# Optimization experiments

Measured on AMD Instinct MI355X. Metric: run time of the kernel, lower is better.

Reference implementation:

```python
import jax, jax.numpy as jnp
import numpy as np

N = 50000      # nodes
E = 800000     # edges
NF = 16        # nfeature_dim
H = 128        # hidden_dim
OUT = 4        # output_dim


def _edge_conv(x, edge_index, W1, b1, W2, b2, aggr):
    """PyG EdgeConv: message = MLP(cat[x_i, x_j - x_i]) per edge, aggregate at target i.
    edge_index[0]=source j, edge_index[1]=target i."""
    src, dst = edge_index[0], edge_index[1]
    xi = x[dst]                                   # [E, F]
    xj = x[src]                                   # [E, F]
    h = jnp.concatenate([xi, xj - xi], axis=-1)   # [E, 2F]
    m = jax.nn.relu(h @ W1 + b1) @ W2 + b2        # [E, H]
    if aggr == 'max':
        out = jax.ops.segment_max(m, dst, num_segments=N)
        out = jnp.where(jnp.isfinite(out), out, 0.0)  # nodes with no in-edges -> 0
    else:  # mean
        s = jax.ops.segment_sum(m, dst, num_segments=N)
        cnt = jax.ops.segment_sum(jnp.ones((m.shape[0], 1), m.dtype), dst, num_segments=N)
        out = s / jnp.maximum(cnt, 1.0)
    return out


def setup_inputs() -> dict:
    key = jax.random.key(0)
    ks = jax.random.split(key, 20)
    s = 0.05
    inp = {
        'x': jax.random.normal(ks[0], (N, NF), dtype=jnp.float32),
        'edge_attr': jax.random.uniform(ks[1], (E, 1), dtype=jnp.float32) + 0.1,
        'edge_index': jax.random.randint(ks[2], (2, E), 0, N, dtype=jnp.int64),
        # conv0: Linear(2*NF->H), Linear(H->H)
        'W01': jax.random.normal(ks[3], (2 * NF, H), dtype=jnp.float32) * s,
        'b01': jnp.zeros((H,), jnp.float32),
        'W02': jax.random.normal(ks[4], (H, H), dtype=jnp.float32) * s,
        'b02': jnp.zeros((H,), jnp.float32),
        # conv1: Linear(2*H->H), Linear(H->H)
        'W11': jax.random.normal(ks[5], (2 * H, H), dtype=jnp.float32) * s,
        'b11': jnp.zeros((H,), jnp.float32),
        'W12': jax.random.normal(ks[6], (H, H), dtype=jnp.float32) * s,
        'b12': jnp.zeros((H,), jnp.float32),
        # conv2: Linear(2*H->H), Linear(H->H)
        'W21': jax.random.normal(ks[7], (2 * H, H), dtype=jnp.float32) * s,
        'b21': jnp.zeros((H,), jnp.float32),
        'W22': jax.random.normal(ks[8], (H, H), dtype=jnp.float32) * s,
        'b22': jnp.zeros((H,), jnp.float32),
        # final fc
        'Wf': jax.random.normal(ks[9], (H, OUT), dtype=jnp.float32) * s,
        'bf': jnp.zeros((OUT,), jnp.float32),
    }
    return inp


def reference(x, edge_attr, edge_index, W01, b01, W02, b02, W11, b11, W12, b12,
              W21, b21, W22, b22, Wf, bf):
    # edge_attr is only nan-checked in the original forward; unused in math.
    # dropout_rate = 0.0 -> identity (eval-mode reference).
    h = _edge_conv(x, edge_index, W01, b01, W02, b02, 'max')
    h = jax.nn.relu(h)
    h = _edge_conv(h, edge_index, W11, b11, W12, b12, 'mean')
    h = jax.nn.relu(h)
    h = _edge_conv(h, edge_index, W21, b21, W22, b22, 'mean')
    return h @ Wf + bf  # [N, OUT]
```

## Files before the change

### kernel.cpp

```cpp
#include <hip/hip_runtime.h>
#include <stdint.h>

#define NNODES 50000
#define NEDGES 800000
#define FDIM 16
#define HDIM 128
#define NPAD 50176
#define NCH 98
#define NBLK64 782

typedef __attribute__((ext_vector_type(8))) short short8;
typedef __attribute__((ext_vector_type(4))) float f32x4;

static constexpr size_t NH  = (size_t)NNODES * HDIM;
static constexpr size_t NHB = NH * sizeof(float);

static constexpr size_t OFF_BUF0  = 0;
static constexpr size_t OFF_BUF1  = NHB;
static constexpr size_t OFF_BUF2  = 2 * NHB;
static constexpr size_t OFF_BFB   = 3 * NHB;
static constexpr size_t OFF_CNT   = OFF_BFB + NH * 2;
static constexpr size_t OFF_CUR   = OFF_CNT + NPAD * 4;
static constexpr size_t OFF_CSUM  = OFF_CUR + NPAD * 4;
static constexpr size_t OFF_COFF  = OFF_CSUM + 512;
static constexpr size_t OFF_WFOLD = OFF_COFF + 512;
static constexpr size_t OFF_BFOLD = OFF_WFOLD + 2048;
static constexpr size_t OFF_FLAG  = OFF_BFOLD + 256;
static constexpr size_t OFF_SSRC  = OFF_FLAG + 256;
static constexpr size_t OFF_SDST  = OFF_SSRC + (size_t)NEDGES * 4;
static constexpr size_t OFF_W02H  = OFF_SDST + (size_t)NEDGES * 4;
static constexpr size_t OFF_W02L  = OFF_W02H + 32768;
static constexpr size_t OFF_W12H  = OFF_W02L + 32768;
static constexpr size_t OFF_W12L  = OFF_W12H + 32768;
static constexpr size_t OFF_W11H  = OFF_W12L + 32768;
static constexpr size_t OFF_W11L  = OFF_W11H + 65536;
static constexpr size_t OFF_W21H  = OFF_W11L + 65536;
static constexpr size_t OFF_W21L  = OFF_W21H + 65536;

__device__ inline unsigned enc_f32(float m) {
  unsigned u = __float_as_uint(m);
  return (u & 0x80000000u) ? ~u : (u | 0x80000000u);
}

__device__ inline ushort bf16_rne(float v) {
  const unsigned u = __float_as_uint(v);
  return (ushort)((u + 0x7fffu + ((u >> 16) & 1u)) >> 16);
}

__device__ inline void bf16_split(float v, ushort& h, ushort& l) {
  unsigned u = __float_as_uint(v);
  unsigned hb = (u + 0x7fffu + ((u >> 16) & 1u)) & 0xffff0000u;
  h = (ushort)(hb >> 16);
  float r = v - __uint_as_float(hb);
  unsigned ur = __float_as_uint(r);
  l = (ushort)((ur + 0x7fffu + ((ur >> 16) & 1u)) >> 16);
}

__device__ inline void split8_tr(const float v[8], short8& hv, short8& lv) {
  unsigned hp[4], lp[4];
  #pragma unroll
  for (int k = 0; k < 4; ++k) {
    const unsigned u0 = __float_as_uint(v[2 * k]);
    const unsigned u1 = __float_as_uint(v[2 * k + 1]);
    const unsigned h0 = u0 & 0xffff0000u;
    const unsigned h1 = u1 & 0xffff0000u;
    const float r0 = v[2 * k]     - __uint_as_float(h0);
    const float r1 = v[2 * k + 1] - __uint_as_float(h1);
    hp[k] = h1 | (h0 >> 16);
    lp[k] = (__float_as_uint(r1) & 0xffff0000u) | (__float_as_uint(r0) >> 16);
  }
  hv = *(short8*)hp;
  lv = *(short8*)lp;
}

__global__ __launch_bounds__(256) void k_init(const int* __restrict__ raw,
                                              int* __restrict__ flag,
                                              unsigned* __restrict__ cnt) {
  const int i = blockIdx.x * 256 + threadIdx.x;
  cnt[i] = 0u;
  if (blockIdx.x == 0 && threadIdx.x == 0) {
    int is64 = 1;
    #pragma unroll
    for (int k = 1; k < 64; k += 2)
      if (raw[k] != 0) is64 = 0;
    *flag = is64;
  }
}

__global__ __launch_bounds__(256) void k_count(const int* __restrict__ raw,
                                               const int* __restrict__ flag,
                                               unsigned* __restrict__ cnt) {
  const size_t e = (size_t)blockIdx.x * 256 + threadIdx.x;
  const int d = (*flag) ? raw[2 * ((size_t)NEDGES + e)] : raw[NEDGES + e];
  atomicAdd(&cnt[d], 1u);
}

__global__ __launch_bounds__(256) void k_scan1(const unsigned* __restrict__ cnt,
                                               unsigned* __restrict__ csum) {
  __shared__ unsigned s[256];
  const int t = threadIdx.x, b = blockIdx.x;
  s[t] = cnt[b * 512 + t] + cnt[b * 512 + 256 + t];
  __syncthreads();
  for (int off = 128; off; off >>= 1) {
    if (t < off) s[t] += s[t + off];
    __syncthreads();
  }
  if (t == 0) csum[b] = s[0];
}

__global__ void k_scan2(const unsigned* __restrict__ csum,
                        unsigned* __restrict__ coff) {
  if (threadIdx.x == 0) {
    unsigned r = 0;
    for (int i = 0; i < NCH; ++i) { coff[i] = r; r += csum[i]; }
  }
}

__global__ __launch_bounds__(256) void k_scan3(const unsigned* __restrict__ cnt,
                                               const unsigned* __restrict__ coff,
                                               unsigned* __restrict__ cursor) {
  __shared__ unsigned s[256];
  const int t = threadIdx.x, b = blockIdx.x;
  const int base = b * 512;
  const unsigned c0 = cnt[base + 2 * t], c1 = cnt[base + 2 * t + 1];
  s[t] = c0 + c1;
  __syncthreads();
  for (int off = 1; off < 256; off <<= 1) {
    unsigned v = s[t];
    if (t >= off) v += s[t - off];
    __syncthreads();
    s[t] = v;
    __syncthreads();
  }
  const unsigned o = coff[b] + s[t] - (c0 + c1);
  cursor[base + 2 * t] = o;
  cursor[base + 2 * t + 1] = o + c0;
}

__global__ __launch_bounds__(256) void k_scatter(const int* __restrict__ raw,
                                                 const int* __restrict__ flag,
                                                 unsigned* __restrict__ cursor,
                                                 int* __restrict__ ssrc,
                                                 int* __restrict__ sdst) {
  const size_t e = (size_t)blockIdx.x * 256 + threadIdx.x;
  int s, d;
  if (*flag) { s = raw[2 * e]; d = raw[2 * ((size_t)NEDGES + e)]; }
  else       { s = raw[e];     d = raw[NEDGES + e]; }
  const unsigned p = atomicAdd(&cursor[d], 1u);
  ssrc[p] = s;
  sdst[p] = d;
}

__device__ inline void prepw_body(const float* __restrict__ W2,
                                  ushort* __restrict__ Whi,
                                  ushort* __restrict__ Wlo, int blk) {
  const int gid = blk * 256 + threadIdx.x;
  const int row = gid & 15;
  const int kg  = (gid >> 4) & 3;
  const int ks  = (gid >> 6) & 3;
  const int ct  = gid >> 8;
  const int col = ct * 16 + row;
  const int k0  = ks * 32 + kg * 8;
  short8 hv, lv;
  #pragma unroll
  for (int j = 0; j < 8; ++j) {
    ushort h, l;
    bf16_split(W2[(size_t)(k0 + j) * HDIM + col], h, l);
    hv[j] = (short)h; lv[j] = (short)l;
  }
  *(short8*)(Whi + (size_t)gid * 8) = hv;
  *(short8*)(Wlo + (size_t)gid * 8) = lv;
}

__device__ inline void packab_body(const float* __restrict__ W1,
                                   ushort* __restrict__ Whi,
                                   ushort* __restrict__ Wlo, int blk) {
  const int gid = blk * 256 + threadIdx.x;
  const int row = gid & 15;
  const int kg  = (gid >> 4) & 3;
  const int ks  = (gid >> 6) & 3;
  const int ct  = gid >> 8;
  const int col = ct * 16 + row;
  const int k0  = ks * 32 + kg * 8;
  short8 hv, lv;
  #pragma unroll
  for (int j = 0; j < 8; ++j) {
    const int k = k0 + j;
    float v;
    if (col < HDIM) v = W1[(size_t)k * HDIM + col] - W1[(size_t)(k + HDIM) * HDIM + col];
    else            v = W1[(size_t)(k + HDIM) * HDIM + (col - HDIM)];
    ushort h, l;
    bf16_split(v, h, l);
    hv[j] = (short)h; lv[j] = (short)l;
  }
  *(short8*)(Whi + (size_t)gid * 8) = hv;
  *(short8*)(Wlo + (size_t)gid * 8) = lv;
}

__global__ __launch_bounds__(256) void k_prep_all(
    const float* __restrict__ W02, const float* __restrict__ W12,
    const float* __restrict__ W11, const float* __restrict__ W21,
    const float* __restrict__ W22, const float* __restrict__ Wf,
    const float* __restrict__ b22, const float* __restrict__ bf,
    ushort* __restrict__ W02h, ushort* __restrict__ W02l,
    ushort* __restrict__ W12h, ushort* __restrict__ W12l,
    ushort* __restrict__ W11h, ushort* __restrict__ W11l,
    ushort* __restrict__ W21h, ushort* __restrict__ W21l,
    float* __restrict__ Wfold, float* __restrict__ bfold) {
  const int b = blockIdx.x;
  if (b < 8)       prepw_body(W02, W02h, W02l, b);
  else if (b < 16) prepw_body(W12, W12h, W12l, b - 8);
  else if (b < 32) packab_body(W11, W11h, W11l, b - 16);
  else if (b < 48) packab_body(W21, W21h, W21l, b - 32);
  else {
    const int t = (b - 48) * 256 + threadIdx.x;
    const int f = t >> 2, o = t & 3;
    float acc = 0.f;
    for (int h = 0; h < HDIM; ++h)
      acc = fmaf(W22[f * HDIM + h], Wf[h * 4 + o], acc);
    Wfold[t] = acc;
    if (t < 4) {
      float a = bf[t];
      for (int h = 0; h < HDIM; ++h) a = fmaf(b22[h], Wf[h * 4 + t], a);
      bfold[t] = a;
    }
  }
}

__global__ __launch_bounds__(256) void k_node_ab16(const float* __restrict__ x,
                                                   const float* __restrict__ W1,
                                                   const float* __restrict__ b1,
                                                   float* __restrict__ A,
                                                   ushort* __restrict__ Bb) {
  __shared__ float s_x[16 * FDIM];
  const int tid = threadIdx.x;
  const int nb = blockIdx.x * 16;
  s_x[tid] = x[(size_t)nb * FDIM + tid];
  __syncthreads();
  const int h = tid & 127;
  const int half = tid >> 7;
  float accA[8], accB[8];
  #pragma unroll
  for (int j = 0; j < 8; ++j) { accA[j] = 0.f; accB[j] = 0.f; }
  #pragma unroll 4
  for (int f = 0; f < FDIM; ++f) {
    const float wt = W1[f * HDIM + h];
    const float wb = W1[(f + FDIM) * HDIM + h];
    const float wd = wt - wb;
    #pragma unroll
    for (int j = 0; j < 8; ++j) {
      const float xv = s_x[(half * 8 + j) * FDIM + f];
      accA[j] = fmaf(xv, wd, accA[j]);
      accB[j] = fmaf(xv, wb, accB[j]);
    }
  }
  const float bias = b1[h];
  #pragma unroll
  for (int j = 0; j < 8; ++j) {
    const size_t idx = (size_t)(nb + half * 8 + j) * HDIM + h;
    A[idx] = accA[j] + bias;
    Bb[idx] = bf16_rne(accB[j]);
  }
}

__global__ __launch_bounds__(256) void k_node_ab_mfma(
    const unsigned* __restrict__ X, const ushort* __restrict__ Whi,
    const ushort* __restrict__ Wlo, const float* __restrict__ b1,
    float* __restrict__ A, ushort* __restrict__ Bb) {
  __shared__ __align__(16) ushort s_hi[64 * 128];
  __shared__ __align__(16) ushort s_lo[64 * 128];
  const int tid = threadIdx.x;
  const int nb = blockIdx.x * 64;

  #pragma unroll
  for (int it = 0; it < 4; ++it) {
    const int idx = tid + it * 256;
    const int row = idx >> 4;
    const int kg8 = idx & 15;
    const int n = nb + row;
    float v[8];
    if (n < NNODES) {
      const unsigned* p = X + (size_t)n * HDIM + kg8 * 8;
      const uint4 u0 = *(const uint4*)p;
      const uint4 u1 = *(const uint4*)(p + 4);
      const unsigned uu[8] = {u0.x, u0.y, u0.z, u0.w, u1.x, u1.y, u1.z, u1.w};
      #pragma unroll
      for (int j = 0; j < 8; ++j)
        v[j] = (uu[j] & 0x80000000u) ? __uint_as_float(uu[j] ^ 0x80000000u) : 0.f;
    } else {
      #pragma unroll
      for (int j = 0; j < 8; ++j) v[j] = 0.f;
    }
    short8 hv, lv;
    split8_tr(v, hv, lv);
    const int unit = row * 16 + (kg8 ^ (row & 15));
    *(short8*)(s_hi + unit * 8) = hv;
    *(short8*)(s_lo + unit * 8) = lv;
  }
  __syncthreads();

  const int l15 = tid & 15;
  const int l4  = (tid >> 4) & 3;
  const int w   = tid >> 6;

  f32x4 acc[4][4];
  #pragma unroll
  for (int rt = 0; rt < 4; ++rt)
    #pragma unroll
    for (int c = 0; c < 4; ++c)
      #pragma unroll
      for (int r = 0; r < 4; ++r) acc[rt][c][r] = 0.f;

  #pragma unroll
  for (int ks = 0; ks < 4; ++ks) {
    short8 wh[4], wl[4];
    #pragma unroll
    for (int ctl = 0; ctl < 4; ++ctl) {
      const int ct_g = w * 4 + ctl;
      const size_t u = ((size_t)(((ct_g * 4 + ks) * 4 + l4) * 16 + l15)) * 8;
      wh[ctl] = *(const short8*)(Whi + u);
      wl[ctl] = *(const short8*)(Wlo + u);
    }
    #pragma unroll
    for (int rt = 0; rt < 4; ++rt) {
      const int unit = (rt * 16 + l15) * 16 + ((ks * 4 + l4) ^ l15);
      const short8 ah = *(const short8*)(s_hi + unit * 8);
      const short8 al = *(const short8*)(s_lo + unit * 8);
      #pragma unroll
      for (int ctl = 0; ctl < 4; ++ctl) {
        acc[rt][ctl] = __builtin_amdgcn_mfma_f32_16x16x32_bf16(al, wh[ctl], acc[rt][ctl], 0, 0, 0);
        acc[rt][ctl] = __builtin_amdgcn_mfma_f32_16x16x32_bf16(ah, wl[ctl], acc[rt][ctl], 0, 0, 0);
        acc[rt][ctl] = __builtin_amdgcn_mfma_f32_16x16x32_bf16(ah, wh[ctl], acc[rt][ctl], 0, 0, 0);
      }
    }
  }

  #pragma unroll
  for (int ctl = 0; ctl < 4; ++ctl) {
    const int col_g = w * 64 + ctl * 16 + l15;
    if (col_g < HDIM) {
      const float bias = b1[col_g];
      #pragma unroll
      for (int rt = 0; rt < 4; ++rt)
        #pragma unroll
        for (int r = 0; r < 4; ++r) {
          const int n = nb + rt * 16 + l4 * 4 + r;
          if (n < NNODES) A[(size_t)n * HDIM + col_g] = acc[rt][ctl][r] + bias;
        }
    } else {
      const int cb = col_g - HDIM;
      #pragma unroll
      for (int rt = 0; rt < 4; ++rt)
        #pragma unroll
        for (int r = 0; r < 4; ++r) {
          const int n = nb + rt * 16 + l4 * 4 + r;
          if (n < NNODES) Bb[(size_t)n * HDIM + cb] = bf16_rne(acc[rt][ctl][r]);
        }
    }
  }
}

__global__ __launch_bounds__(256) void k_node_l2_fused(
    const float* __restrict__ S, const unsigned* __restrict__ cnt,
    const ushort* __restrict__ W12h, const ushort* __restrict__ W12l,
    const float* __restrict__ b12,
    const ushort* __restrict__ W21h, const ushort* __restrict__ W21l,
    const float* __restrict__ b21,
    float* __restrict__ A, ushort* __restrict__ Bb) {
  __shared__ __align__(16) ushort s_hi[64 * 128];
  __shared__ __align__(16) ushort s_lo[64 * 128];
  __shared__ float s_m[64 * 132];
  __shared__ float s_scale[64];
  __shared__ float s_alive[64];
  const int tid = threadIdx.x;
  const int nb = blockIdx.x * 64;
  if (tid < 64) {
    const int n = nb + tid;
    const unsigned c = (n < NNODES) ? cnt[n] : 0u;
    s_scale[tid] = c ? 1.f / (float)c : 0.f;
    s_alive[tid] = c ? 1.f : 0.f;
  }
  __syncthreads();

  #pragma unroll
  for (int it = 0; it < 4; ++it) {
    const int idx = tid + it * 256;
    const int row = idx >> 4;
    const int kg8 = idx & 15;
    const int n = nb + row;
    float v[8];
    if (n < NNODES) {
      const float sc = s_scale[row];
      const float* p = S + (size_t)n * HDIM + kg8 * 8;
      const float4 a0 = *(const float4*)p;
      const float4 a1 = *(const float4*)(p + 4);
      v[0] = a0.x * sc; v[1] = a0.y * sc; v[2] = a0.z * sc; v[3] = a0.w * sc;
      v[4] = a1.x * sc; v[5] = a1.y * sc; v[6] = a1.z * sc; v[7] = a1.w * sc;
    } else {
      #pragma unroll
      for (int j = 0; j < 8; ++j) v[j] = 0.f;
    }
    short8 hv, lv;
    split8_tr(v, hv, lv);
    const int unit = row * 16 + (kg8 ^ (row & 15));
    *(short8*)(s_hi + unit * 8) = hv;
    *(short8*)(s_lo + unit * 8) = lv;
  }
  __syncthreads();

  const int l15 = tid & 15;
  const int l4  = (tid >> 4) & 3;
  const int w   = tid >> 6;

  {
    f32x4 acc[4][2];
    #pragma unroll
    for (int rt = 0; rt < 4; ++rt)
      #pragma unroll
      for (int c = 0; c < 2; ++c)
        #pragma unroll
        for (int r = 0; r < 4; ++r) acc[rt][c][r] = 0.f;

    #pragma unroll
    for (int ks = 0; ks < 4; ++ks) {
      short8 wh[2], wl[2];
      #pragma unroll
      for (int ctl = 0; ctl < 2; ++ctl) {
        const int ct_g = w * 2 + ctl;
        const size_t u = ((size_t)(((ct_g * 4 + ks) * 4 + l4) * 16 + l15)) * 8;
        wh[ctl] = *(const short8*)(W12h + u);
        wl[ctl] = *(const short8*)(W12l + u);
      }
      #pragma unroll
      for (int rt = 0; rt < 4; ++rt) {
        const int unit = (rt * 16 + l15) * 16 + ((ks * 4 + l4) ^ l15);
        const short8 ah = *(const short8*)(s_hi + unit * 8);
        const short8 al = *(const short8*)(s_lo + unit * 8);
        #pragma unroll
        for (int ctl = 0; ctl < 2; ++ctl) {
          acc[rt][ctl] = __builtin_amdgcn_mfma_f32_16x16x32_bf16(al, wh[ctl], acc[rt][ctl], 0, 0, 0);
          acc[rt][ctl] = __builtin_amdgcn_mfma_f32_16x16x32_bf16(ah, wl[ctl], acc[rt][ctl], 0, 0, 0);
          acc[rt][ctl] = __builtin_amdgcn_mfma_f32_16x16x32_bf16(ah, wh[ctl], acc[rt][ctl], 0, 0, 0);
        }
      }
    }

    const float bb0 = b12[w * 32 + l15];
    const float bb1 = b12[w * 32 + 16 + l15];
    #pragma unroll
    for (int rt = 0; rt < 4; ++rt)
      #pragma unroll
      for (int ctl = 0; ctl < 2; ++ctl)
        #pragma unroll
        for (int r = 0; r < 4; ++r) {
          const int row = rt * 16 + l4 * 4 + r;
          s_m[row * 132 + w * 32 + ctl * 16 + l15] =
              fmaxf(acc[rt][ctl][r] + (ctl ? bb1 : bb0), 0.f) * s_alive[row];
        }
  }
  __syncthreads();

  #pragma unroll
  for (int it = 0; it < 4; ++it) {
    const int idx = tid + it * 256;
    const int row = idx >> 4;
    const int kg8 = idx & 15;
    const float* p = s_m + row * 132 + kg8 * 8;
    float v[8];
    const float4 a0 = *(const float4*)p;
    const float4 a1 = *(const float4*)(p + 4);
    v[0] = a0.x; v[1] = a0.y; v[2] = a0.z; v[3] = a0.w;
    v[4] = a1.x; v[5] = a1.y; v[6] = a1.z; v[7] = a1.w;
    short8 hv, lv;
    split8_tr(v, hv, lv);
    const int unit = row * 16 + (kg8 ^ (row & 15));
    *(short8*)(s_hi + unit * 8) = hv;
    *(short8*)(s_lo + unit * 8) = lv;
  }
  __syncthreads();

  f32x4 acc2[4][4];
  #pragma unroll
  for (int rt = 0; rt < 4; ++rt)
    #pragma unroll
    for (int c = 0; c < 4; ++c)
      #pragma unroll
      for (int r = 0; r < 4; ++r) acc2[rt][c][r] = 0.f;

  #pragma unroll
  for (int ks = 0; ks < 4; ++ks) {
    short8 wh[4], wl[4];
    #pragma unroll
    for (int ctl = 0; ctl < 4; ++ctl) {
      const int ct_g = w * 4 + ctl;
      const size_t u = ((size_t)(((ct_g * 4 + ks) * 4 + l4) * 16 + l15)) * 8;
      wh[ctl] = *(const short8*)(W21h + u);
      wl[ctl] = *(const short8*)(W21l + u);
    }
    #pragma unroll
    for (int rt = 0; rt < 4; ++rt) {
      const int unit = (rt * 16 + l15) * 16 + ((ks * 4 + l4) ^ l15);
      const short8 ah = *(const short8*)(s_hi + unit * 8);
      const short8 al = *(const short8*)(s_lo + unit * 8);
      #pragma unroll
      for (int ctl = 0; ctl < 4; ++ctl) {
        acc2[rt][ctl] = __builtin_amdgcn_mfma_f32_16x16x32_bf16(al, wh[ctl], acc2[rt][ctl], 0, 0, 0);
        acc2[rt][ctl] = __builtin_amdgcn_mfma_f32_16x16x32_bf16(ah, wl[ctl], acc2[rt][ctl], 0, 0, 0);
        acc2[rt][ctl] = __builtin_amdgcn_mfma_f32_16x16x32_bf16(ah, wh[ctl], acc2[rt][ctl], 0, 0, 0);
      }
    }
  }

  #pragma unroll
  for (int ctl = 0; ctl < 4; ++ctl) {
    const int col_g = w * 64 + ctl * 16 + l15;
    if (col_g < HDIM) {
      const float bias = b21[col_g];
      #pragma unroll
      for (int rt = 0; rt < 4; ++rt)
        #pragma unroll
        for (int r = 0; r < 4; ++r) {
          const int n = nb + rt * 16 + l4 * 4 + r;
          if (n < NNODES) A[(size_t)n * HDIM + col_g] = acc2[rt][ctl][r] + bias;
        }
    } else {
      const int cb = col_g - HDIM;
      #pragma unroll
      for (int rt = 0; rt < 4; ++rt)
        #pragma unroll
        for (int r = 0; r < 4; ++r) {
          const int n = nb + rt * 16 + l4 * 4 + r;
          if (n < NNODES) Bb[(size_t)n * HDIM + cb] = bf16_rne(acc2[rt][ctl][r]);
        }
    }
  }
}

__global__ __launch_bounds__(256) void k_edge_l0_mfma(
    const float* __restrict__ A0, const ushort* __restrict__ B0b,
    const int* __restrict__ ssrc, const int* __restrict__ sdst,
    const ushort* __restrict__ Whi, const ushort* __restrict__ Wlo,
    const float* __restrict__ b2, unsigned* __restrict__ outenc) {
  __shared__ __align__(16) char s_un[4 * 64 * 33 * 4];
  __shared__ int s_dstA[64];
  __shared__ int s_srcA[64];
  ushort* s_thi = (ushort*)s_un;
  ushort* s_tlo = (ushort*)(s_un + 16384);
  float*  s_m   = (float*)s_un;

  const int tid = threadIdx.x;
  const int eb = blockIdx.x * 64;
  if (tid < 64) s_dstA[tid] = sdst[eb + tid];
  else if (tid < 128) s_srcA[tid - 64] = ssrc[eb + tid - 64];
  __syncthreads();

  #pragma unroll
  for (int it = 0; it < 4; ++it) {
    const int idx = tid + it * 256;
    const int e = idx >> 4;
    const int kg8 = idx & 15;
    const int k0 = kg8 * 8;
    const float* ap = A0 + (size_t)s_dstA[e] * HDIM + k0;
    const ushort* bp = B0b + (size_t)s_srcA[e] * HDIM + k0;
    const float4 a0 = *(const float4*)ap;
    const float4 a1 = *(const float4*)(ap + 4);
    const short8 b8 = *(const short8*)bp;
    const float af[8] = {a0.x, a0.y, a0.z, a0.w, a1.x, a1.y, a1.z, a1.w};
    float v[8];
    #pragma unroll
    for (int j = 0; j < 8; ++j) {
      const float bv = __uint_as_float(((unsigned)(ushort)b8[j]) << 16);
      v[j] = fmaxf(af[j] + bv, 0.f);
    }
    short8 hv, lv;
    split8_tr(v, hv, lv);
    const int unit = e * 16 + (kg8 ^ (e & 15));
    *(short8*)(s_thi + unit * 8) = hv;
    *(short8*)(s_tlo + unit * 8) = lv;
  }
  __syncthreads();

  const int l15 = tid & 15;
  const int l4  = (tid >> 4) & 3;
  const int w   = tid >> 6;

  f32x4 acc[4][2];
  #pragma unroll
  for (int rt = 0; rt < 4; ++rt)
    #pragma unroll
    for (int c = 0; c < 2; ++c)
      #pragma unroll
      for (int r = 0; r < 4; ++r) acc[rt][c][r] = 0.f;

  #pragma unroll
  for (int ks = 0; ks < 4; ++ks) {
    short8 wh[2], wl[2];
    #pragma unroll
    for (int ctl = 0; ctl < 2; ++ctl) {
      const int ct_g = w * 2 + ctl;
      const size_t u = ((size_t)(((ct_g * 4 + ks) * 4 + l4) * 16 + l15)) * 8;
      wh[ctl] = *(const short8*)(Whi + u);
      wl[ctl] = *(const short8*)(Wlo + u);
    }
    #pragma unroll
    for (int rt = 0; rt < 4; ++rt) {
      const int e = rt * 16 + l15;
      const int unit = e * 16 + ((ks * 4 + l4) ^ l15);
      const short8 ah = *(const short8*)(s_thi + unit * 8);
      const short8 al = *(const short8*)(s_tlo + unit * 8);
      #pragma unroll
      for (int ctl = 0; ctl < 2; ++ctl) {
        acc[rt][ctl] = __builtin_amdgcn_mfma_f32_16x16x32_bf16(al, wh[ctl], acc[rt][ctl], 0, 0, 0);
        acc[rt][ctl] = __builtin_amdgcn_mfma_f32_16x16x32_bf16(ah, wl[ctl], acc[rt][ctl], 0, 0, 0);
        acc[rt][ctl] = __builtin_amdgcn_mfma_f32_16x16x32_bf16(ah, wh[ctl], acc[rt][ctl], 0, 0, 0);
      }
    }
  }
  __syncthreads();

  const float bb0 = b2[w * 32 + l15];
  const float bb1 = b2[w * 32 + 16 + l15];
  float* sm = s_m + w * (64 * 33);
  #pragma unroll
  for (int rt = 0; rt < 4; ++rt)
    #pragma unroll
    for (int ctl = 0; ctl < 2; ++ctl)
      #pragma unroll
      for (int r = 0; r < 4; ++r)
        sm[(rt * 16 + l4 * 4 + r) * 33 + ctl * 16 + l15] =
            acc[rt][ctl][r] + (ctl ? bb1 : bb0);
  __syncthreads();

  {
    const int l = tid & 63;
    const int col = l & 31;
    const int g = l >> 5;
    const int e0 = g * 32;
    int curd = s_dstA[e0];
    float run = sm[e0 * 33 + col];
    for (int e = e0 + 1; e < e0 + 32; ++e) {
      const int d = s_dstA[e];
      const float v = sm[e * 33 + col];
      if (d == curd) run = fmaxf(run, v);
      else {
        atomicMax(outenc + (size_t)curd * HDIM + w * 32 + col, enc_f32(run));
        curd = d; run = v;
      }
    }
    atomicMax(outenc + (size_t)curd * HDIM + w * 32 + col, enc_f32(run));
  }
}

__global__ __launch_bounds__(256) void k_seg_mean(const float* __restrict__ A,
                                                  const ushort* __restrict__ B,
                                                  const int* __restrict__ ssrc,
                                                  const unsigned* __restrict__ endv,
                                                  const unsigned* __restrict__ cnt,
                                                  float* __restrict__ S) {
  const int tid = threadIdx.x;
  const int n = blockIdx.x * 4 + (tid >> 6);
  const int lane = tid & 63;
  const unsigned end = endv[n];
  unsigned e = end - cnt[n];
  const float2 a = *(const float2*)(A + (size_t)n * HDIM + lane * 2);
  float sx = 0.f, sy = 0.f;
  for (; e + 8 <= end; e += 8) {
    int s[8];
    #pragma unroll
    for (int k = 0; k < 8; ++k) s[k] = ssrc[e + k];
    unsigned bv[8];
    #pragma unroll
    for (int k = 0; k < 8; ++k)
      bv[k] = *(const unsigned*)(B + (size_t)s[k] * HDIM + lane * 2);
    #pragma unroll
    for (int k = 0; k < 8; ++k) {
      sx += fmaxf(a.x + __uint_as_float(bv[k] << 16), 0.f);
      sy += fmaxf(a.y + __uint_as_float(bv[k] & 0xffff0000u), 0.f);
    }
  }
  for (; e < end; ++e) {
    const unsigned bv = *(const unsigned*)(B + (size_t)ssrc[e] * HDIM + lane * 2);
    sx += fmaxf(a.x + __uint_as_float(bv << 16), 0.f);
    sy += fmaxf(a.y + __uint_as_float(bv & 0xffff0000u), 0.f);
  }
  float2 o; o.x = sx; o.y = sy;
  *(float2*)(S + (size_t)n * HDIM + lane * 2) = o;
}

__global__ __launch_bounds__(256) void k_seg_final(const float* __restrict__ A,
                                                   const ushort* __restrict__ B,
                                                   const int* __restrict__ ssrc,
                                                   const unsigned* __restrict__ endv,
                                                   const unsigned* __restrict__ cnt,
                                                   const float* __restrict__ Wfold,
                                                   const float* __restrict__ bfold,
                                                   const float* __restrict__ bf,
                                                   float* __restrict__ out) {
  const int tid = threadIdx.x;
  const int n = blockIdx.x * 4 + (tid >> 6);
  const int lane = tid & 63;
  const unsigned deg = cnt[n];
  if (deg == 0) {
    if (lane == 0) {
      float4 o; o.x = bf[0]; o.y = bf[1]; o.z = bf[2]; o.w = bf[3];
      ((float4*)out)[n] = o;
    }
    return;
  }
  const unsigned end = endv[n];
  unsigned e = end - deg;
  const float2 a = *(const float2*)(A + (size_t)n * HDIM + lane * 2);
  float sx = 0.f, sy = 0.f;
  for (; e + 8 <= end; e += 8) {
    int s[8];
    #pragma unroll
    for (int k = 0; k < 8; ++k) s[k] = ssrc[e + k];
    unsigned bv[8];
    #pragma unroll
    for (int k = 0; k < 8; ++k)
      bv[k] = *(const unsigned*)(B + (size_t)s[k] * HDIM + lane * 2);
    #pragma unroll
    for (int k = 0; k < 8; ++k) {
      sx += fmaxf(a.x + __uint_as_float(bv[k] << 16), 0.f);
      sy += fmaxf(a.y + __uint_as_float(bv[k] & 0xffff0000u), 0.f);
    }
  }
  for (; e < end; ++e) {
    const unsigned bv = *(const unsigned*)(B + (size_t)ssrc[e] * HDIM + lane * 2);
    sx += fmaxf(a.x + __uint_as_float(bv << 16), 0.f);
    sy += fmaxf(a.y + __uint_as_float(bv & 0xffff0000u), 0.f);
  }
  const float inv = 1.f / (float)deg;
  const float vx = sx * inv, vy = sy * inv;
  const float4 w0 = ((const float4*)Wfold)[lane * 2];
  const float4 w1 = ((const float4*)Wfold)[lane * 2 + 1];
  float p0 = fmaf(vx, w0.x, vy * w1.x);
  float p1 = fmaf(vx, w0.y, vy * w1.y);
  float p2 = fmaf(vx, w0.z, vy * w1.z);
  float p3 = fmaf(vx, w0.w, vy * w1.w);
  #pragma unroll
  for (int off = 32; off; off >>= 1) {
    p0 += __shfl_xor(p0, off);
    p1 += __shfl_xor(p1, off);
    p2 += __shfl_xor(p2, off);
    p3 += __shfl_xor(p3, off);
  }
  if (lane == 0) {
    float4 o;
    o.x = p0 + bfold[0]; o.y = p1 + bfold[1];
    o.z = p2 + bfold[2]; o.w = p3 + bfold[3];
    ((float4*)out)[n] = o;
  }
}

extern "C" void kernel_launch(void* const* d_in, const int* in_sizes, int n_in,
                              void* d_out, int out_size, void* d_ws, size_t ws_size,
                              hipStream_t stream) {
  const float* x   = (const float*)d_in[0];
  const int*   eidx = (const int*)d_in[2];
  const float* W01 = (const float*)d_in[3];
  const float* b01 = (const float*)d_in[4];
  const float* W02 = (const float*)d_in[5];
  const float* b02 = (const float*)d_in[6];
  const float* W11 = (const float*)d_in[7];
  const float* b11 = (const float*)d_in[8];
  const float* W12 = (const float*)d_in[9];
  const float* b12 = (const float*)d_in[10];
  const float* W21 = (const float*)d_in[11];
  const float* b21 = (const float*)d_in[12];
  const float* W22 = (const float*)d_in[13];
  const float* b22 = (const float*)d_in[14];
  const float* Wf  = (const float*)d_in[15];
  const float* bf  = (const float*)d_in[16];
  float* out = (float*)d_out;
  char* ws = (char*)d_ws;

  float* buf0 = (float*)(ws + OFF_BUF0);
  float* buf1 = (float*)(ws + OFF_BUF1);
  float* buf2 = (float*)(ws + OFF_BUF2);
  ushort* bufB = (ushort*)(ws + OFF_BFB);
  unsigned* cnt    = (unsigned*)(ws + OFF_CNT);
  unsigned* cursor = (unsigned*)(ws + OFF_CUR);
  unsigned* csum   = (unsigned*)(ws + OFF_CSUM);
  unsigned* coff   = (unsigned*)(ws + OFF_COFF);
  float* Wfold = (float*)(ws + OFF_WFOLD);
  float* bfold = (float*)(ws + OFF_BFOLD);
  int* flag  = (int*)(ws + OFF_FLAG);
  int* ssrc  = (int*)(ws + OFF_SSRC);
  int* sdst  = (int*)(ws + OFF_SDST);
  ushort* W02h = (ushort*)(ws + OFF_W02H);
  ushort* W02l = (ushort*)(ws + OFF_W02L);
  ushort* W12h = (ushort*)(ws + OFF_W12H);
  ushort* W12l = (ushort*)(ws + OFF_W12L);
  ushort* W11h = (ushort*)(ws + OFF_W11H);
  ushort* W11l = (ushort*)(ws + OFF_W11L);
  ushort* W21h = (ushort*)(ws + OFF_W21H);
  ushort* W21l = (ushort*)(ws + OFF_W21L);

  k_init<<<NPAD / 256, 256, 0, stream>>>(eidx, flag, cnt);
  k_count<<<NEDGES / 256, 256, 0, stream>>>(eidx, flag, cnt);
  k_scan1<<<NCH, 256, 0, stream>>>(cnt, csum);
  k_scan2<<<1, 64, 0, stream>>>(csum, coff);
  k_scan3<<<NCH, 256, 0, stream>>>(cnt, coff, cursor);
  k_scatter<<<NEDGES / 256, 256, 0, stream>>>(eidx, flag, cursor, ssrc, sdst);
  k_prep_all<<<50, 256, 0, stream>>>(W02, W12, W11, W21, W22, Wf, b22, bf,
                                     W02h, W02l, W12h, W12l, W11h, W11l,
                                     W21h, W21l, Wfold, bfold);

  k_node_ab16<<<NNODES / 16, 256, 0, stream>>>(x, W01, b01, buf0, bufB);
  hipMemsetAsync(buf2, 0, NHB, stream);
  k_edge_l0_mfma<<<NEDGES / 64, 256, 0, stream>>>(buf0, bufB, ssrc, sdst,
                                                  W02h, W02l, b02, (unsigned*)buf2);

  k_node_ab_mfma<<<NBLK64, 256, 0, stream>>>((const unsigned*)buf2, W11h, W11l,
                                             b11, buf0, bufB);
  k_seg_mean<<<NNODES / 4, 256, 0, stream>>>(buf0, bufB, ssrc, cursor, cnt, buf1);

  k_node_l2_fused<<<NBLK64, 256, 0, stream>>>(buf1, cnt, W12h, W12l, b12,
                                              W21h, W21l, b21, buf0, bufB);
  k_seg_final<<<NNODES / 4, 256, 0, stream>>>(buf0, bufB, ssrc, cursor, cnt,
                                              Wfold, bfold, bf, out);

  (void)in_sizes; (void)n_in; (void)out_size; (void)ws_size;
}
```

Baseline: 468.3 us.

## Use single-pass bf16 MFMA in layer-0 edge kernel, fuse memset, deepen gather unroll

The layer-0 edge MLP second matmul drops the split hi/lo bf16 three-MFMA emulation of fp32 and uses one bf16 MFMA, with activations converted by a packed bf16 convert instruction. This cuts MFMA work and shared-memory traffic to a third but lowers precision of the max-aggregated messages. The separate memset of the max-aggregation buffer is folded into the init kernel, and the mean-aggregation gather loops are unrolled from 8 to 16 edges, with a 4-edge remainder step in one of them.

```diff
diff --git a/kernel.cpp b/kernel.cpp
--- a/kernel.cpp
+++ b/kernel.cpp
@@ -73,12 +73,22 @@
   lv = *(short8*)lp;
 }
 
+__device__ inline short8 cvtpk8_bf16(const float v[8]) {
+  unsigned r[4];
+  #pragma unroll
+  for (int k = 0; k < 4; ++k)
+    asm("v_cvt_pk_bf16_f32 %0, %1, %2" : "=v"(r[k]) : "v"(v[2 * k]), "v"(v[2 * k + 1]));
+  return *(short8*)r;
+}
+
 __global__ __launch_bounds__(256) void k_init(const int* __restrict__ raw,
                                               int* __restrict__ flag,
-                                              unsigned* __restrict__ cnt) {
+                                              unsigned* __restrict__ cnt,
+                                              unsigned* __restrict__ outenc) {
   const int i = blockIdx.x * 256 + threadIdx.x;
-  cnt[i] = 0u;
-  if (blockIdx.x == 0 && threadIdx.x == 0) {
+  outenc[i] = 0u;
+  if (i < NPAD) cnt[i] = 0u;
+  if (i == 0) {
     int is64 = 1;
     #pragma unroll
     for (int k = 1; k < 64; k += 2)
@@ -539,14 +549,13 @@
 __global__ __launch_bounds__(256) void k_edge_l0_mfma(
     const float* __restrict__ A0, const ushort* __restrict__ B0b,
     const int* __restrict__ ssrc, const int* __restrict__ sdst,
-    const ushort* __restrict__ Whi, const ushort* __restrict__ Wlo,
+    const ushort* __restrict__ Whi,
     const float* __restrict__ b2, unsigned* __restrict__ outenc) {
   __shared__ __align__(16) char s_un[4 * 64 * 33 * 4];
   __shared__ int s_dstA[64];
   __shared__ int s_srcA[64];
-  ushort* s_thi = (ushort*)s_un;
-  ushort* s_tlo = (ushort*)(s_un + 16384);
-  float*  s_m   = (float*)s_un;
+  ushort* s_t = (ushort*)s_un;
+  float*  s_m = (float*)s_un;
 
   const int tid = threadIdx.x;
   const int eb = blockIdx.x * 64;
@@ -572,11 +581,9 @@
       const float bv = __uint_as_float(((unsigned)(ushort)b8[j]) << 16);
       v[j] = fmaxf(af[j] + bv, 0.f);
     }
-    short8 hv, lv;
-    split8_tr(v, hv, lv);
+    const short8 hv = cvtpk8_bf16(v);
     const int unit = e * 16 + (kg8 ^ (e & 15));
-    *(short8*)(s_thi + unit * 8) = hv;
-    *(short8*)(s_tlo + unit * 8) = lv;
+    *(short8*)(s_t + unit * 8) = hv;
   }
   __syncthreads();
 
@@ -594,26 +601,21 @@
 
   #pragma unroll
   for (int ks = 0; ks < 4; ++ks) {
-    short8 wh[2], wl[2];
+    short8 wh[2];
     #pragma unroll
     for (int ctl = 0; ctl < 2; ++ctl) {
       const int ct_g = w * 2 + ctl;
       const size_t u = ((size_t)(((ct_g * 4 + ks) * 4 + l4) * 16 + l15)) * 8;
       wh[ctl] = *(const short8*)(Whi + u);
-      wl[ctl] = *(const short8*)(Wlo + u);
     }
     #pragma unroll
     for (int rt = 0; rt < 4; ++rt) {
       const int e = rt * 16 + l15;
       const int unit = e * 16 + ((ks * 4 + l4) ^ l15);
-      const short8 ah = *(const short8*)(s_thi + unit * 8);
-      const short8 al = *(const short8*)(s_tlo + unit * 8);
-      #pragma unroll
-      for (int ctl = 0; ctl < 2; ++ctl) {
-        acc[rt][ctl] = __builtin_amdgcn_mfma_f32_16x16x32_bf16(al, wh[ctl], acc[rt][ctl], 0, 0, 0);
-        acc[rt][ctl] = __builtin_amdgcn_mfma_f32_16x16x32_bf16(ah, wl[ctl], acc[rt][ctl], 0, 0, 0);
+      const short8 ah = *(const short8*)(s_t + unit * 8);
+      #pragma unroll
+      for (int ctl = 0; ctl < 2; ++ctl)
         acc[rt][ctl] = __builtin_amdgcn_mfma_f32_16x16x32_bf16(ah, wh[ctl], acc[rt][ctl], 0, 0, 0);
-      }
     }
   }
   __syncthreads();
@@ -664,16 +666,30 @@
   unsigned e = end - cnt[n];
   const float2 a = *(const float2*)(A + (size_t)n * HDIM + lane * 2);
   float sx = 0.f, sy = 0.f;
-  for (; e + 8 <= end; e += 8) {
-    int s[8];
-    #pragma unroll
-    for (int k = 0; k < 8; ++k) s[k] = ssrc[e + k];
-    unsigned bv[8];
-    #pragma unroll
-    for (int k = 0; k < 8; ++k)
+  for (; e + 16 <= end; e += 16) {
+    int s[16];
+    #pragma unroll
+    for (int k = 0; k < 16; ++k) s[k] = ssrc[e + k];
+    unsigned bv[16];
+    #pragma unroll
+    for (int k = 0; k < 16; ++k)
       bv[k] = *(const unsigned*)(B + (size_t)s[k] * HDIM + lane * 2);
     #pragma unroll
-    for (int k = 0; k < 8; ++k) {
+    for (int k = 0; k < 16; ++k) {
+      sx += fmaxf(a.x + __uint_as_float(bv[k] << 16), 0.f);
+      sy += fmaxf(a.y + __uint_as_float(bv[k] & 0xffff0000u), 0.f);
+    }
+  }
+  for (; e + 4 <= end; e += 4) {
+    int s[4];
+    #pragma unroll
+    for (int k = 0; k < 4; ++k) s[k] = ssrc[e + k];
+    unsigned bv[4];
+    #pragma unroll
+    for (int k = 0; k < 4; ++k)
+      bv[k] = *(const unsigned*)(B + (size_t)s[k] * HDIM + lane * 2);
+    #pragma unroll
+    for (int k = 0; k < 4; ++k) {
       sx += fmaxf(a.x + __uint_as_float(bv[k] << 16), 0.f);
       sy += fmaxf(a.y + __uint_as_float(bv[k] & 0xffff0000u), 0.f);
     }
@@ -711,16 +727,16 @@
   unsigned e = end - deg;
   const float2 a = *(const float2*)(A + (size_t)n * HDIM + lane * 2);
   float sx = 0.f, sy = 0.f;
-  for (; e + 8 <= end; e += 8) {
-    int s[8];
-    #pragma unroll
-    for (int k = 0; k < 8; ++k) s[k] = ssrc[e + k];
-    unsigned bv[8];
-    #pragma unroll
-    for (int k = 0; k < 8; ++k)
+  for (; e + 16 <= end; e += 16) {
+    int s[16];
+    #pragma unroll
+    for (int k = 0; k < 16; ++k) s[k] = ssrc[e + k];
+    unsigned bv[16];
+    #pragma unroll
+    for (int k = 0; k < 16; ++k)
       bv[k] = *(const unsigned*)(B + (size_t)s[k] * HDIM + lane * 2);
     #pragma unroll
-    for (int k = 0; k < 8; ++k) {
+    for (int k = 0; k < 16; ++k) {
       sx += fmaxf(a.x + __uint_as_float(bv[k] << 16), 0.f);
       sy += fmaxf(a.y + __uint_as_float(bv[k] & 0xffff0000u), 0.f);
     }
@@ -797,7 +813,7 @@
   ushort* W21h = (ushort*)(ws + OFF_W21H);
   ushort* W21l = (ushort*)(ws + OFF_W21L);
 
-  k_init<<<NPAD / 256, 256, 0, stream>>>(eidx, flag, cnt);
+  k_init<<<(int)(NH / 256), 256, 0, stream>>>(eidx, flag, cnt, (unsigned*)buf2);
   k_count<<<NEDGES / 256, 256, 0, stream>>>(eidx, flag, cnt);
   k_scan1<<<NCH, 256, 0, stream>>>(cnt, csum);
   k_scan2<<<1, 64, 0, stream>>>(csum, coff);
@@ -808,9 +824,8 @@
                                      W21h, W21l, Wfold, bfold);
 
   k_node_ab16<<<NNODES / 16, 256, 0, stream>>>(x, W01, b01, buf0, bufB);
-  hipMemsetAsync(buf2, 0, NHB, stream);
   k_edge_l0_mfma<<<NEDGES / 64, 256, 0, stream>>>(buf0, bufB, ssrc, sdst,
-                                                  W02h, W02l, b02, (unsigned*)buf2);
+                                                  W02h, b02, (unsigned*)buf2);
 
   k_node_ab_mfma<<<NBLK64, 256, 0, stream>>>((const unsigned*)buf2, W11h, W11l,
                                              b11, buf0, bufB);
```

After: 470.1 us. About the same (+0.4%).
